# Performance work log

Hardware: AMD Instinct MI355X
Metric: run time of the kernel (lower is better)

## Reference

```python
import jax, jax.numpy as jnp
import numpy as np

HIDDEN = 2048
INTER = 5632
N_EXPERTS = 8
TOP_K = 2


def setup_inputs() -> dict:
    key = jax.random.key(0)
    ks = jax.random.split(key, 6)
    x = jax.random.normal(ks[0], (4, 2048, HIDDEN), dtype=jnp.float32)
    router_w = jax.random.normal(ks[1], (N_EXPERTS, HIDDEN), dtype=jnp.float32) * 0.02
    router_b = jnp.zeros((N_EXPERTS,), dtype=jnp.float32)
    Wg = jax.random.normal(ks[2], (N_EXPERTS, INTER, HIDDEN), dtype=jnp.float32) * 0.02
    Wu = jax.random.normal(ks[3], (N_EXPERTS, INTER, HIDDEN), dtype=jnp.float32) * 0.02
    Wd = jax.random.normal(ks[4], (N_EXPERTS, HIDDEN, INTER), dtype=jnp.float32) * 0.02
    return {"x": x, "router_w": router_w, "router_b": router_b, "Wg": Wg, "Wu": Wu, "Wd": Wd}


def reference(x, router_w, router_b, Wg, Wu, Wd):
    batch_shape = x.shape[:-1]
    xf = x.reshape(-1, HIDDEN)  # [T, H]
    T = xf.shape[0]

    # Router: softmax -> top-k -> renormalize (matches torch forward)
    logits = xf @ router_w.T + router_b            # [T, E]
    probs = jax.nn.softmax(logits, axis=-1)
    w, idx = jax.lax.top_k(probs, TOP_K)           # [T, K]
    w = w / jnp.sum(w, axis=-1, keepdims=True)

    # Dense combine weights [T, E]: zero where expert not selected.
    combine = jnp.zeros((T, N_EXPERTS), dtype=xf.dtype)
    combine = combine.at[jnp.arange(T)[:, None], idx].set(w)

    # Weighted sum of SwiGLU expert outputs (loop over fixed small E).
    out = jnp.zeros_like(xf)
    for e in range(N_EXPERTS):
        g = jax.nn.silu(xf @ Wg[e].T)              # [T, I]
        u = xf @ Wu[e].T                           # [T, I]
        h = (g * u) @ Wd[e].T                      # [T, H]
        out = out + combine[:, e:e + 1] * h
    return out.reshape(*batch_shape, HIDDEN)
```

## Files before the change

### kernel.cpp

```cpp
#include <hip/hip_runtime.h>
#include <stdint.h>

#define HID 2048
#define ITR 5632
#define NE 8
#define TT 8192

typedef __attribute__((ext_vector_type(4))) float f4;
typedef __attribute__((ext_vector_type(8))) short s8v;
typedef __attribute__((ext_vector_type(4))) float acc4;
typedef __attribute__((ext_vector_type(4))) unsigned short u4v;
typedef __attribute__((ext_vector_type(8))) unsigned short u8v;
typedef unsigned short ushort_t;

__device__ __forceinline__ unsigned short f2bf(float f) {
    union { float f; uint32_t u; } v; v.f = f;
    uint32_t u = v.u;
    return (unsigned short)((u + 0x7FFFu + ((u >> 16) & 1u)) >> 16);
}

__device__ __forceinline__ void gload16(const unsigned short* g, unsigned short* l) {
    __builtin_amdgcn_global_load_lds(
        (const __attribute__((address_space(1))) unsigned int*)g,
        (__attribute__((address_space(3))) unsigned int*)l, 16, 0, 0);
}

__device__ __forceinline__ int lby(int row, int s) {
    return row * 64 + ((s ^ ((row >> 1) & 3)) * 16);
}

__global__ __launch_bounds__(256) void k_cvt(const float* __restrict__ src,
                                             unsigned short* __restrict__ dst) {
    size_t i = ((size_t)blockIdx.x * 256 + threadIdx.x) * 8;
    f4 a = *(const f4*)(src + i);
    f4 b = *(const f4*)(src + i + 4);
    u8v o;
    o[0]=f2bf(a.x); o[1]=f2bf(a.y); o[2]=f2bf(a.z); o[3]=f2bf(a.w);
    o[4]=f2bf(b.x); o[5]=f2bf(b.y); o[6]=f2bf(b.z); o[7]=f2bf(b.w);
    *(u8v*)(dst + i) = o;
}

#define WBLK 45056
__global__ __launch_bounds__(256) void k_cvtW(const float* __restrict__ a,
                                              const float* __restrict__ b,
                                              const float* __restrict__ c,
                                              unsigned short* __restrict__ oa,
                                              unsigned short* __restrict__ ob,
                                              unsigned short* __restrict__ oc) {
    int bb = blockIdx.x;
    const float* s; unsigned short* d;
    if (bb < WBLK)            { s = a; d = oa; }
    else if (bb < 2 * WBLK)   { s = b; d = ob; bb -= WBLK; }
    else                      { s = c; d = oc; bb -= 2 * WBLK; }
    size_t i = ((size_t)bb * 256 + threadIdx.x) * 8;
    f4 va = *(const f4*)(s + i);
    f4 vb = *(const f4*)(s + i + 4);
    u8v o;
    o[0]=f2bf(va.x); o[1]=f2bf(va.y); o[2]=f2bf(va.z); o[3]=f2bf(va.w);
    o[4]=f2bf(vb.x); o[5]=f2bf(vb.y); o[6]=f2bf(vb.z); o[7]=f2bf(vb.w);
    *(u8v*)(d + i) = o;
}

__global__ __launch_bounds__(256) void k_router(const float* __restrict__ x,
                                                const float* __restrict__ rw,
                                                const float* __restrict__ rb,
                                                int* __restrict__ cnt,
                                                int* __restrict__ tokL,
                                                int* __restrict__ slotL,
                                                float* __restrict__ gateL) {
    int lane = threadIdx.x & 63;
    int wv = threadIdx.x >> 6;
    int t = blockIdx.x * 4 + wv;
    const float* xr = x + (size_t)t * HID;
    float acc[NE];
    #pragma unroll
    for (int e = 0; e < NE; ++e) acc[e] = 0.f;
    #pragma unroll
    for (int i = 0; i < 8; ++i) {
        f4 xv = *(const f4*)(xr + i * 256 + lane * 4);
        #pragma unroll
        for (int e = 0; e < NE; ++e) {
            f4 wv4 = *(const f4*)(rw + e * HID + i * 256 + lane * 4);
            acc[e] += xv.x * wv4.x + xv.y * wv4.y + xv.z * wv4.z + xv.w * wv4.w;
        }
    }
    #pragma unroll
    for (int off = 32; off; off >>= 1)
        #pragma unroll
        for (int e = 0; e < NE; ++e) acc[e] += __shfl_xor(acc[e], off, 64);
    if (lane == 0) {
        float lg[NE];
        #pragma unroll
        for (int e = 0; e < NE; ++e) lg[e] = acc[e] + rb[e];
        int i1 = 0;
        #pragma unroll
        for (int e = 1; e < NE; ++e) if (lg[e] > lg[i1]) i1 = e;
        int i2 = -1;
        #pragma unroll
        for (int e = 0; e < NE; ++e) {
            if (e == i1) continue;
            if (i2 < 0 || lg[e] > lg[i2]) i2 = e;
        }
        float ex = __expf(lg[i2] - lg[i1]);
        float w1 = 1.f / (1.f + ex);
        float w2 = ex / (1.f + ex);
        int p = atomicAdd(&cnt[i1], 1);
        tokL[i1 * TT + p] = t; slotL[i1 * TT + p] = t * 2;     gateL[i1 * TT + p] = w1;
        p = atomicAdd(&cnt[i2], 1);
        tokL[i2 * TT + p] = t; slotL[i2 * TT + p] = t * 2 + 1; gateL[i2 * TT + p] = w2;
    }
}


__global__ __launch_bounds__(512, 2) void k_g1p(const unsigned short* __restrict__ xb,
                                                const unsigned short* __restrict__ WgB,
                                                const unsigned short* __restrict__ WuB,
                                                const int* __restrict__ cnt,
                                                const int* __restrict__ tokL,
                                                const int* __restrict__ slotL,
                                                unsigned short* __restrict__ Hb) {
    int bx = blockIdx.x;
    int e = bx / (32 * 44);
    int r = bx % (32 * 44);
    int mt = r / 44, nt = r % 44;
    int M = cnt[e];
    int m0 = mt * 256;
    if (m0 >= M) return;
    int n0 = nt * 128;

    __shared__ __align__(16) unsigned short lds[65536];
    __shared__ int sTok[256];
    __shared__ int sSlot[256];

    int tid = threadIdx.x;
    if (tid < 256) {
        int m = m0 + tid;
        int mc = m < M ? m : M - 1;
        sTok[tid]  = tokL[e * TT + mc];
        sSlot[tid] = slotL[e * TT + mc];
    }
    __syncthreads();

    int wv = tid >> 6, lane = tid & 63;
    int lrow = lane >> 2;
    int slog = (lane & 3) ^ ((lane >> 3) & 3);

    const unsigned short* aS0 = xb + (size_t)sTok[(2 * wv) * 16 + lrow] * HID + slog * 8;
    const unsigned short* aS1 = xb + (size_t)sTok[(2 * wv + 1) * 16 + lrow] * HID + slog * 8;
    const unsigned short* gS  = WgB + ((size_t)e * ITR + n0 + wv * 16 + lrow) * HID + slog * 8;
    const unsigned short* uS  = WuB + ((size_t)e * ITR + n0 + wv * 16 + lrow) * HID + slog * 8;

    unsigned short* ldsA = lds;
    unsigned short* ldsG = lds + 32768;
    unsigned short* ldsU = lds + 49152;

    auto STAGE = [&](int reg, int kh) {
        int ko = kh * 32;
        gload16(aS0 + ko, ldsA + reg * 8192 + (2 * wv) * 512);
        gload16(aS1 + ko, ldsA + reg * 8192 + (2 * wv + 1) * 512);
        gload16(gS + ko,  ldsG + reg * 4096 + wv * 512);
        gload16(uS + ko,  ldsU + reg * 4096 + wv * 512);
    };

    int wr = wv >> 2, wc = wv & 3;
    int lr = lane & 15, ls = lane >> 4;

    int aOff[8], gOff[2], uOff[2];
    #pragma unroll
    for (int mi = 0; mi < 8; ++mi) aOff[mi] = lby(wr * 128 + mi * 16 + lr, ls);
    #pragma unroll
    for (int ni = 0; ni < 2; ++ni) {
        gOff[ni] = 65536 + lby(wc * 32 + ni * 16 + lr, ls);
        uOff[ni] = 98304 + lby(wc * 32 + ni * 16 + lr, ls);
    }

    acc4 zero4 = {0.f, 0.f, 0.f, 0.f};
    acc4 ag[8][2], au[8][2];
    #pragma unroll
    for (int mi = 0; mi < 8; ++mi)
        #pragma unroll
        for (int ni = 0; ni < 2; ++ni) { ag[mi][ni] = zero4; au[mi][ni] = zero4; }

    STAGE(0, 0); STAGE(1, 1); STAGE(2, 2); STAGE(3, 3);
    asm volatile("s_waitcnt vmcnt(12)" ::: "memory");
    __builtin_amdgcn_s_barrier();

    #pragma unroll 4
    for (int h = 0; h < 64; ++h) {
        int reg = h & 3;
        const char* baseA = (const char*)lds + reg * 16384;
        const char* baseB = (const char*)lds + reg * 8192;
        s8v af[8], gf[2], uf[2];
        #pragma unroll
        for (int mi = 0; mi < 8; ++mi) af[mi] = *(const s8v*)(baseA + aOff[mi]);
        #pragma unroll
        for (int ni = 0; ni < 2; ++ni) {
            gf[ni] = *(const s8v*)(baseB + gOff[ni]);
            uf[ni] = *(const s8v*)(baseB + uOff[ni]);
        }
        asm volatile("s_waitcnt lgkmcnt(0)" ::: "memory");
        __builtin_amdgcn_sched_barrier(0);
        __builtin_amdgcn_s_barrier();
        __builtin_amdgcn_sched_barrier(0);
        int kh = h + 4 < 64 ? h + 4 : 63;
        STAGE(reg, kh);
        __builtin_amdgcn_s_setprio(1);
        #pragma unroll
        for (int mi = 0; mi < 8; ++mi)
            #pragma unroll
            for (int ni = 0; ni < 2; ++ni) {
                ag[mi][ni] = __builtin_amdgcn_mfma_f32_16x16x32_bf16(af[mi], gf[ni], ag[mi][ni], 0, 0, 0);
                au[mi][ni] = __builtin_amdgcn_mfma_f32_16x16x32_bf16(af[mi], uf[ni], au[mi][ni], 0, 0, 0);
            }
        __builtin_amdgcn_s_setprio(0);
        asm volatile("s_waitcnt vmcnt(12)" ::: "memory");
        __builtin_amdgcn_s_barrier();
    }
    asm volatile("s_waitcnt vmcnt(0)" ::: "memory");

    #pragma unroll
    for (int mi = 0; mi < 8; ++mi) {
        #pragma unroll
        for (int j = 0; j < 4; ++j) {
            int m = wr * 128 + mi * 16 + ls * 4 + j;
            if (m0 + m < M) {
                size_t rowOff = (size_t)sSlot[m] * ITR + n0 + wc * 32 + lr;
                #pragma unroll
                for (int ni = 0; ni < 2; ++ni) {
                    float g = ag[mi][ni][j], u = au[mi][ni][j];
                    float h2 = g * (1.f / (1.f + __expf(-g))) * u;
                    Hb[rowOff + ni * 16] = f2bf(h2);
                }
            }
        }
    }
}

__global__ __launch_bounds__(512, 2) void k_g2p(const unsigned short* __restrict__ Hb,
                                                const unsigned short* __restrict__ WdB,
                                                const int* __restrict__ cnt,
                                                const int* __restrict__ tokL,
                                                const int* __restrict__ slotL,
                                                const float* __restrict__ gateL,
                                                float* __restrict__ out) {
    int bx = blockIdx.x;
    int e = bx / (32 * 8);
    int r = bx % (32 * 8);
    int mt = r / 8, nt = r % 8;
    int M = cnt[e];
    int m0 = mt * 256;
    if (m0 >= M) return;
    int n0 = nt * 256;

    __shared__ __align__(16) unsigned short lds[65536];
    __shared__ int sTok[256];
    __shared__ int sSlot[256];
    __shared__ float sGate[256];

    int tid = threadIdx.x;
    if (tid < 256) {
        int m = m0 + tid;
        int mc = m < M ? m : M - 1;
        sTok[tid]  = tokL[e * TT + mc];
        sSlot[tid] = slotL[e * TT + mc];
        sGate[tid] = gateL[e * TT + mc];
    }
    __syncthreads();

    int wv = tid >> 6, lane = tid & 63;
    int lrow = lane >> 2;
    int slog = (lane & 3) ^ ((lane >> 3) & 3);

    const unsigned short* aS0 = Hb + (size_t)sSlot[(2 * wv) * 16 + lrow] * ITR + slog * 8;
    const unsigned short* aS1 = Hb + (size_t)sSlot[(2 * wv + 1) * 16 + lrow] * ITR + slog * 8;
    const unsigned short* bS0 = WdB + ((size_t)e * HID + n0 + (2 * wv) * 16 + lrow) * ITR + slog * 8;
    const unsigned short* bS1 = WdB + ((size_t)e * HID + n0 + (2 * wv + 1) * 16 + lrow) * ITR + slog * 8;

    unsigned short* ldsA = lds;
    unsigned short* ldsB = lds + 32768;

    auto STAGE = [&](int reg, int kh) {
        int ko = kh * 32;
        gload16(aS0 + ko, ldsA + reg * 8192 + (2 * wv) * 512);
        gload16(aS1 + ko, ldsA + reg * 8192 + (2 * wv + 1) * 512);
        gload16(bS0 + ko, ldsB + reg * 8192 + (2 * wv) * 512);
        gload16(bS1 + ko, ldsB + reg * 8192 + (2 * wv + 1) * 512);
    };

    int wr = wv >> 2, wc = wv & 3;
    int lr = lane & 15, ls = lane >> 4;

    int aOff[8], bOff[4];
    #pragma unroll
    for (int mi = 0; mi < 8; ++mi) aOff[mi] = lby(wr * 128 + mi * 16 + lr, ls);
    #pragma unroll
    for (int ni = 0; ni < 4; ++ni) bOff[ni] = 65536 + lby(wc * 64 + ni * 16 + lr, ls);

    acc4 zero4 = {0.f, 0.f, 0.f, 0.f};
    acc4 a4[8][4];
    #pragma unroll
    for (int mi = 0; mi < 8; ++mi)
        #pragma unroll
        for (int ni = 0; ni < 4; ++ni) a4[mi][ni] = zero4;

    STAGE(0, 0); STAGE(1, 1); STAGE(2, 2); STAGE(3, 3);
    asm volatile("s_waitcnt vmcnt(12)" ::: "memory");
    __builtin_amdgcn_s_barrier();

    #pragma unroll 4
    for (int h = 0; h < 176; ++h) {
        int reg = h & 3;
        const char* base = (const char*)lds + reg * 16384;
        s8v af[8], bf[4];
        #pragma unroll
        for (int mi = 0; mi < 8; ++mi) af[mi] = *(const s8v*)(base + aOff[mi]);
        #pragma unroll
        for (int ni = 0; ni < 4; ++ni) bf[ni] = *(const s8v*)(base + bOff[ni]);
        asm volatile("s_waitcnt lgkmcnt(0)" ::: "memory");
        __builtin_amdgcn_sched_barrier(0);
        __builtin_amdgcn_s_barrier();
        __builtin_amdgcn_sched_barrier(0);
        int kh = h + 4 < 176 ? h + 4 : 175;
        STAGE(reg, kh);
        __builtin_amdgcn_s_setprio(1);
        #pragma unroll
        for (int mi = 0; mi < 8; ++mi)
            #pragma unroll
            for (int ni = 0; ni < 4; ++ni)
                a4[mi][ni] = __builtin_amdgcn_mfma_f32_16x16x32_bf16(af[mi], bf[ni], a4[mi][ni], 0, 0, 0);
        __builtin_amdgcn_s_setprio(0);
        asm volatile("s_waitcnt vmcnt(12)" ::: "memory");
        __builtin_amdgcn_s_barrier();
    }
    asm volatile("s_waitcnt vmcnt(0)" ::: "memory");

    #pragma unroll
    for (int mi = 0; mi < 8; ++mi) {
        #pragma unroll
        for (int j = 0; j < 4; ++j) {
            int m = wr * 128 + mi * 16 + ls * 4 + j;
            if (m0 + m < M) {
                int t = sTok[m];
                float w = sGate[m];
                float* orow = out + (size_t)t * HID + n0 + wc * 64 + lr;
                #pragma unroll
                for (int ni = 0; ni < 4; ++ni)
                    atomicAdd(orow + ni * 16, w * a4[mi][ni][j]);
            }
        }
    }
}

#define BM 128
#define BN 128
#define BK 64
#define MT1 64
#define NT1 44
#define NT2 16

__global__ __launch_bounds__(256) void k_gemm1(const unsigned short* __restrict__ xb,
                                               const float* __restrict__ Wg,
                                               const float* __restrict__ Wu,
                                               const int* __restrict__ cnt,
                                               const int* __restrict__ tokL,
                                               const int* __restrict__ slotL,
                                               unsigned short* __restrict__ Hb) {
    int bx = blockIdx.x;
    int e = bx / (MT1 * NT1);
    int r = bx % (MT1 * NT1);
    int mt = r / NT1, nt = r % NT1;
    int M = cnt[e];
    int m0 = mt * BM;
    if (m0 >= M) return;
    int n0 = nt * BN;

    __shared__ __align__(16) unsigned short lA[BM * BK];
    __shared__ __align__(16) unsigned short lBg[BN * BK];
    __shared__ __align__(16) unsigned short lBu[BN * BK];
    __shared__ int sTok[BM];
    __shared__ int sSlot[BM];

    int tid = threadIdx.x;
    if (tid < BM) {
        int m = m0 + tid;
        int mc = m < M ? m : M - 1;
        sTok[tid] = tokL[e * TT + mc];
        sSlot[tid] = slotL[e * TT + mc];
    }
    __syncthreads();

    int ar = tid >> 3, ac = tid & 7;
    const unsigned short* aP[4];
    #pragma unroll
    for (int i = 0; i < 4; ++i)
        aP[i] = xb + (size_t)sTok[ar + 32 * i] * HID + ac * 8;

    int br = tid >> 4, bc = tid & 15;
    const float* gB = Wg + ((size_t)e * ITR + n0) * HID + bc * 4;
    const float* uB = Wu + ((size_t)e * ITR + n0) * HID + bc * 4;

    int wv = tid >> 6, lane = tid & 63;
    int wm = (wv >> 1) * 64, wn = (wv & 1) * 64;
    int lr = lane & 15, lk = (lane >> 4) * 8;

    acc4 zero4 = {0.f, 0.f, 0.f, 0.f};
    acc4 ag[4][4], au[4][4];
    #pragma unroll
    for (int mi = 0; mi < 4; ++mi)
        #pragma unroll
        for (int ni = 0; ni < 4; ++ni) { ag[mi][ni] = zero4; au[mi][ni] = zero4; }

    for (int k0 = 0; k0 < HID; k0 += BK) {
        if (k0) __syncthreads();
        #pragma unroll
        for (int i = 0; i < 4; ++i) {
            int row = ar + 32 * i;
            s8v v = *(const s8v*)(aP[i] + k0);
            int byt = (row * 128 + ac * 16) ^ ((row & 7) << 4);
            *(s8v*)((char*)lA + byt) = v;
        }
        #pragma unroll
        for (int i = 0; i < 8; ++i) {
            int row = br + 16 * i;
            f4 vg = *(const f4*)(gB + (size_t)row * HID + k0);
            f4 vu = *(const f4*)(uB + (size_t)row * HID + k0);
            u4v og = { f2bf(vg.x), f2bf(vg.y), f2bf(vg.z), f2bf(vg.w) };
            u4v ou = { f2bf(vu.x), f2bf(vu.y), f2bf(vu.z), f2bf(vu.w) };
            int byt = (row * 128 + bc * 8) ^ ((row & 7) << 4);
            *(u4v*)((char*)lBg + byt) = og;
            *(u4v*)((char*)lBu + byt) = ou;
        }
        __syncthreads();
        #pragma unroll
        for (int kk = 0; kk < BK; kk += 32) {
            s8v af[4], gf[4], uf[4];
            #pragma unroll
            for (int i = 0; i < 4; ++i) {
                int rowA = wm + i * 16 + lr;
                af[i] = *(const s8v*)((char*)lA + ((rowA * 128 + (kk + lk) * 2) ^ ((rowA & 7) << 4)));
                int rowB = wn + i * 16 + lr;
                int bb = (rowB * 128 + (kk + lk) * 2) ^ ((rowB & 7) << 4);
                gf[i] = *(const s8v*)((char*)lBg + bb);
                uf[i] = *(const s8v*)((char*)lBu + bb);
            }
            #pragma unroll
            for (int mi = 0; mi < 4; ++mi)
                #pragma unroll
                for (int ni = 0; ni < 4; ++ni) {
                    ag[mi][ni] = __builtin_amdgcn_mfma_f32_16x16x32_bf16(af[mi], gf[ni], ag[mi][ni], 0, 0, 0);
                    au[mi][ni] = __builtin_amdgcn_mfma_f32_16x16x32_bf16(af[mi], uf[ni], au[mi][ni], 0, 0, 0);
                }
        }
    }
    #pragma unroll
    for (int mi = 0; mi < 4; ++mi) {
        #pragma unroll
        for (int j = 0; j < 4; ++j) {
            int m = wm + mi * 16 + (lane >> 4) * 4 + j;
            if (m0 + m < M) {
                size_t rowOff = (size_t)sSlot[m] * ITR + n0 + wn + lr;
                #pragma unroll
                for (int ni = 0; ni < 4; ++ni) {
                    float g = ag[mi][ni][j], u = au[mi][ni][j];
                    float h = g * (1.f / (1.f + __expf(-g))) * u;
                    Hb[rowOff + ni * 16] = f2bf(h);
                }
            }
        }
    }
}

__global__ __launch_bounds__(256) void k_gemm2(const unsigned short* __restrict__ Hb,
                                               const float* __restrict__ Wd,
                                               const int* __restrict__ cnt,
                                               const int* __restrict__ tokL,
                                               const int* __restrict__ slotL,
                                               const float* __restrict__ gateL,
                                               float* __restrict__ out) {
    int bx = blockIdx.x;
    int e = bx / (MT1 * NT2);
    int r = bx % (MT1 * NT2);
    int mt = r / NT2, nt = r % NT2;
    int M = cnt[e];
    int m0 = mt * BM;
    if (m0 >= M) return;
    int n0 = nt * BN;

    __shared__ __align__(16) unsigned short lA[BM * BK];
    __shared__ __align__(16) unsigned short lB[BN * BK];
    __shared__ int sTok[BM];
    __shared__ int sSlot[BM];
    __shared__ float sGate[BM];

    int tid = threadIdx.x;
    if (tid < BM) {
        int m = m0 + tid;
        int mc = m < M ? m : M - 1;
        sTok[tid] = tokL[e * TT + mc];
        sSlot[tid] = slotL[e * TT + mc];
        sGate[tid] = gateL[e * TT + mc];
    }
    __syncthreads();

    int ar = tid >> 3, ac = tid & 7;
    const unsigned short* aP[4];
    #pragma unroll
    for (int i = 0; i < 4; ++i)
        aP[i] = Hb + (size_t)sSlot[ar + 32 * i] * ITR + ac * 8;

    int br = tid >> 4, bc = tid & 15;
    const float* dB = Wd + ((size_t)e * HID + n0) * ITR + bc * 4;

    int wv = tid >> 6, lane = tid & 63;
    int wm = (wv >> 1) * 64, wn = (wv & 1) * 64;
    int lr = lane & 15, lk = (lane >> 4) * 8;

    acc4 zero4 = {0.f, 0.f, 0.f, 0.f};
    acc4 a4[4][4];
    #pragma unroll
    for (int mi = 0; mi < 4; ++mi)
        #pragma unroll
        for (int ni = 0; ni < 4; ++ni) a4[mi][ni] = zero4;

    for (int k0 = 0; k0 < ITR; k0 += BK) {
        if (k0) __syncthreads();
        #pragma unroll
        for (int i = 0; i < 4; ++i) {
            int row = ar + 32 * i;
            s8v v = *(const s8v*)(aP[i] + k0);
            int byt = (row * 128 + ac * 16) ^ ((row & 7) << 4);
            *(s8v*)((char*)lA + byt) = v;
        }
        #pragma unroll
        for (int i = 0; i < 8; ++i) {
            int row = br + 16 * i;
            f4 vd = *(const f4*)(dB + (size_t)row * ITR + k0);
            u4v od = { f2bf(vd.x), f2bf(vd.y), f2bf(vd.z), f2bf(vd.w) };
            int byt = (row * 128 + bc * 8) ^ ((row & 7) << 4);
            *(u4v*)((char*)lB + byt) = od;
        }
        __syncthreads();
        #pragma unroll
        for (int kk = 0; kk < BK; kk += 32) {
            s8v af[4], bf[4];
            #pragma unroll
            for (int i = 0; i < 4; ++i) {
                int rowA = wm + i * 16 + lr;
                af[i] = *(const s8v*)((char*)lA + ((rowA * 128 + (kk + lk) * 2) ^ ((rowA & 7) << 4)));
                int rowB = wn + i * 16 + lr;
                bf[i] = *(const s8v*)((char*)lB + ((rowB * 128 + (kk + lk) * 2) ^ ((rowB & 7) << 4)));
            }
            #pragma unroll
            for (int mi = 0; mi < 4; ++mi)
                #pragma unroll
                for (int ni = 0; ni < 4; ++ni)
                    a4[mi][ni] = __builtin_amdgcn_mfma_f32_16x16x32_bf16(af[mi], bf[ni], a4[mi][ni], 0, 0, 0);
        }
    }
    #pragma unroll
    for (int mi = 0; mi < 4; ++mi) {
        #pragma unroll
        for (int j = 0; j < 4; ++j) {
            int m = wm + mi * 16 + (lane >> 4) * 4 + j;
            if (m0 + m < M) {
                int t = sTok[m];
                float w = sGate[m];
                float* orow = out + (size_t)t * HID + n0 + wn + lr;
                #pragma unroll
                for (int ni = 0; ni < 4; ++ni)
                    atomicAdd(orow + ni * 16, w * a4[mi][ni][j]);
            }
        }
    }
}

extern "C" void kernel_launch(void* const* d_in, const int* in_sizes, int n_in,
                              void* d_out, int out_size, void* d_ws, size_t ws_size,
                              hipStream_t stream) {
    const float* x  = (const float*)d_in[0];
    const float* rw = (const float*)d_in[1];
    const float* rb = (const float*)d_in[2];
    const float* Wg = (const float*)d_in[3];
    const float* Wu = (const float*)d_in[4];
    const float* Wd = (const float*)d_in[5];
    float* out = (float*)d_out;
    char* ws = (char*)d_ws;

    const size_t OFF_XB   = 0;
    const size_t OFF_HB   = 33554432ull;
    const size_t OFF_TOK  = 218103808ull;
    const size_t OFF_SLOT = 218365952ull;
    const size_t OFF_GATE = 218628096ull;
    const size_t OFF_CNT  = 218890240ull;
    const size_t OFF_WG   = 218891264ull;
    const size_t OFF_WU   = 403440640ull;
    const size_t OFF_WD   = 587990016ull;
    const size_t NEED     = 772539392ull;

    unsigned short* xb   = (unsigned short*)(ws + OFF_XB);
    unsigned short* Hb   = (unsigned short*)(ws + OFF_HB);
    int*   tokL  = (int*)(ws + OFF_TOK);
    int*   slotL = (int*)(ws + OFF_SLOT);
    float* gateL = (float*)(ws + OFF_GATE);
    int*   cnt   = (int*)(ws + OFF_CNT);

    hipMemsetAsync(cnt, 0, NE * sizeof(int), stream);
    hipMemsetAsync(out, 0, (size_t)out_size * sizeof(float), stream);
    k_cvt<<<8192, 256, 0, stream>>>(x, xb);
    k_router<<<2048, 256, 0, stream>>>(x, rw, rb, cnt, tokL, slotL, gateL);

    if (ws_size >= NEED) {
        unsigned short* WgB = (unsigned short*)(ws + OFF_WG);
        unsigned short* WuB = (unsigned short*)(ws + OFF_WU);
        unsigned short* WdB = (unsigned short*)(ws + OFF_WD);
        k_cvtW<<<3 * WBLK, 256, 0, stream>>>(Wg, Wu, Wd, WgB, WuB, WdB);
        k_g1p<<<NE * 32 * 44, 512, 0, stream>>>(xb, WgB, WuB, cnt, tokL, slotL, Hb);
        k_g2p<<<NE * 32 * 8, 512, 0, stream>>>(Hb, WdB, cnt, tokL, slotL, gateL, out);
    } else {
        k_gemm1<<<NE * MT1 * NT1, 256, 0, stream>>>(xb, Wg, Wu, cnt, tokL, slotL, Hb);
        k_gemm2<<<NE * MT1 * NT2, 256, 0, stream>>>(Hb, Wd, cnt, tokL, slotL, gateL, out);
    }
}
```

Baseline: 1.938 ms.

## Restructure grouped-GEMM pipelines to single-barrier two-ahead prefetch without LDS swizzle

Reworks the k-loop in both grouped expert GEMM kernels. The old loop prefetched four stages ahead with two barriers per iteration. The new loop prefetches two stages ahead into a four-slot ring, issues global-to-LDS loads right after the fragment reads, and keeps one barrier per iteration, with the last two stages peeled out. It also drops the XOR swizzle on the LDS layout in favour of plain row-major offsets, which cuts address math but risks LDS bank conflicts on the fragment reads.

```diff
diff --git a/kernel.cpp b/kernel.cpp
--- a/kernel.cpp
+++ b/kernel.cpp
@@ -11,7 +11,6 @@
 typedef __attribute__((ext_vector_type(4))) float acc4;
 typedef __attribute__((ext_vector_type(4))) unsigned short u4v;
 typedef __attribute__((ext_vector_type(8))) unsigned short u8v;
-typedef unsigned short ushort_t;
 
 __device__ __forceinline__ unsigned short f2bf(float f) {
     union { float f; uint32_t u; } v; v.f = f;
@@ -25,9 +24,7 @@
         (__attribute__((address_space(3))) unsigned int*)l, 16, 0, 0);
 }
 
-__device__ __forceinline__ int lby(int row, int s) {
-    return row * 64 + ((s ^ ((row >> 1) & 3)) * 16);
-}
+#define MFMA16(a, b, c) __builtin_amdgcn_mfma_f32_16x16x32_bf16(a, b, c, 0, 0, 0)
 
 __global__ __launch_bounds__(256) void k_cvt(const float* __restrict__ src,
                                              unsigned short* __restrict__ dst) {
@@ -112,7 +109,7 @@
 }
 
 
-__global__ __launch_bounds__(512, 2) void k_g1p(const unsigned short* __restrict__ xb,
+__global__ __launch_bounds__(512, 2) void k_g1q(const unsigned short* __restrict__ xb,
                                                 const unsigned short* __restrict__ WgB,
                                                 const unsigned short* __restrict__ WuB,
                                                 const int* __restrict__ cnt,
@@ -128,7 +125,7 @@
     if (m0 >= M) return;
     int n0 = nt * 128;
 
-    __shared__ __align__(16) unsigned short lds[65536];
+    __shared__ __align__(16) unsigned short lds[4 * 16384];
     __shared__ int sTok[256];
     __shared__ int sSlot[256];
 
@@ -142,36 +139,24 @@
     __syncthreads();
 
     int wv = tid >> 6, lane = tid & 63;
-    int lrow = lane >> 2;
-    int slog = (lane & 3) ^ ((lane >> 3) & 3);
-
-    const unsigned short* aS0 = xb + (size_t)sTok[(2 * wv) * 16 + lrow] * HID + slog * 8;
-    const unsigned short* aS1 = xb + (size_t)sTok[(2 * wv + 1) * 16 + lrow] * HID + slog * 8;
-    const unsigned short* gS  = WgB + ((size_t)e * ITR + n0 + wv * 16 + lrow) * HID + slog * 8;
-    const unsigned short* uS  = WuB + ((size_t)e * ITR + n0 + wv * 16 + lrow) * HID + slog * 8;
-
-    unsigned short* ldsA = lds;
-    unsigned short* ldsG = lds + 32768;
-    unsigned short* ldsU = lds + 49152;
-
-    auto STAGE = [&](int reg, int kh) {
-        int ko = kh * 32;
-        gload16(aS0 + ko, ldsA + reg * 8192 + (2 * wv) * 512);
-        gload16(aS1 + ko, ldsA + reg * 8192 + (2 * wv + 1) * 512);
-        gload16(gS + ko,  ldsG + reg * 4096 + wv * 512);
-        gload16(uS + ko,  ldsU + reg * 4096 + wv * 512);
-    };
+    int srow = wv * 16 + (lane >> 2);
+    int scol = (lane & 3) * 8;
+    const unsigned short* sA0 = xb + (size_t)sTok[srow] * HID + scol;
+    const unsigned short* sA1 = xb + (size_t)sTok[128 + srow] * HID + scol;
+    const unsigned short* sG  = WgB + ((size_t)e * ITR + n0 + srow) * HID + scol;
+    const unsigned short* sU  = WuB + ((size_t)e * ITR + n0 + srow) * HID + scol;
+    int dstW = wv * 512;
 
     int wr = wv >> 2, wc = wv & 3;
     int lr = lane & 15, ls = lane >> 4;
 
     int aOff[8], gOff[2], uOff[2];
     #pragma unroll
-    for (int mi = 0; mi < 8; ++mi) aOff[mi] = lby(wr * 128 + mi * 16 + lr, ls);
+    for (int mi = 0; mi < 8; ++mi) aOff[mi] = (wr * 128 + mi * 16 + lr) * 32 + ls * 8;
     #pragma unroll
     for (int ni = 0; ni < 2; ++ni) {
-        gOff[ni] = 65536 + lby(wc * 32 + ni * 16 + lr, ls);
-        uOff[ni] = 98304 + lby(wc * 32 + ni * 16 + lr, ls);
+        gOff[ni] = 8192  + (wc * 32 + ni * 16 + lr) * 32 + ls * 8;
+        uOff[ni] = 12288 + (wc * 32 + ni * 16 + lr) * 32 + ls * 8;
     }
 
     acc4 zero4 = {0.f, 0.f, 0.f, 0.f};
@@ -181,42 +166,88 @@
         #pragma unroll
         for (int ni = 0; ni < 2; ++ni) { ag[mi][ni] = zero4; au[mi][ni] = zero4; }
 
-    STAGE(0, 0); STAGE(1, 1); STAGE(2, 2); STAGE(3, 3);
-    asm volatile("s_waitcnt vmcnt(12)" ::: "memory");
+    gload16(sA0,      lds + dstW);
+    gload16(sA1,      lds + 4096 + dstW);
+    gload16(sG,       lds + 8192 + dstW);
+    gload16(sU,       lds + 12288 + dstW);
+    gload16(sA0 + 32, lds + 16384 + dstW);
+    gload16(sA1 + 32, lds + 16384 + 4096 + dstW);
+    gload16(sG  + 32, lds + 16384 + 8192 + dstW);
+    gload16(sU  + 32, lds + 16384 + 12288 + dstW);
+    asm volatile("s_waitcnt vmcnt(4)" ::: "memory");
     __builtin_amdgcn_s_barrier();
-
+    __builtin_amdgcn_sched_barrier(0);
+
+    int kS = 64;
     #pragma unroll 4
-    for (int h = 0; h < 64; ++h) {
-        int reg = h & 3;
-        const char* baseA = (const char*)lds + reg * 16384;
-        const char* baseB = (const char*)lds + reg * 8192;
+    for (int tt = 0; tt < 62; ++tt) {
+        int base = (tt & 3) << 14;
         s8v af[8], gf[2], uf[2];
         #pragma unroll
-        for (int mi = 0; mi < 8; ++mi) af[mi] = *(const s8v*)(baseA + aOff[mi]);
+        for (int mi = 0; mi < 8; ++mi) af[mi] = *(const s8v*)(lds + base + aOff[mi]);
         #pragma unroll
         for (int ni = 0; ni < 2; ++ni) {
-            gf[ni] = *(const s8v*)(baseB + gOff[ni]);
-            uf[ni] = *(const s8v*)(baseB + uOff[ni]);
-        }
-        asm volatile("s_waitcnt lgkmcnt(0)" ::: "memory");
-        __builtin_amdgcn_sched_barrier(0);
+            gf[ni] = *(const s8v*)(lds + base + gOff[ni]);
+            uf[ni] = *(const s8v*)(lds + base + uOff[ni]);
+        }
+        int sb = ((tt + 2) & 3) << 14;
+        gload16(sA0 + kS, lds + sb + dstW);
+        gload16(sA1 + kS, lds + sb + 4096 + dstW);
+        gload16(sG  + kS, lds + sb + 8192 + dstW);
+        gload16(sU  + kS, lds + sb + 12288 + dstW);
+        kS += 32;
+        __builtin_amdgcn_s_setprio(1);
+        #pragma unroll
+        for (int mi = 0; mi < 8; ++mi)
+            #pragma unroll
+            for (int ni = 0; ni < 2; ++ni) {
+                ag[mi][ni] = MFMA16(af[mi], gf[ni], ag[mi][ni]);
+                au[mi][ni] = MFMA16(af[mi], uf[ni], au[mi][ni]);
+            }
+        __builtin_amdgcn_s_setprio(0);
+        asm volatile("s_waitcnt vmcnt(4)" ::: "memory");
         __builtin_amdgcn_s_barrier();
         __builtin_amdgcn_sched_barrier(0);
-        int kh = h + 4 < 64 ? h + 4 : 63;
-        STAGE(reg, kh);
-        __builtin_amdgcn_s_setprio(1);
+    }
+    {
+        int base = 2 << 14;
+        s8v af[8], gf[2], uf[2];
+        #pragma unroll
+        for (int mi = 0; mi < 8; ++mi) af[mi] = *(const s8v*)(lds + base + aOff[mi]);
+        #pragma unroll
+        for (int ni = 0; ni < 2; ++ni) {
+            gf[ni] = *(const s8v*)(lds + base + gOff[ni]);
+            uf[ni] = *(const s8v*)(lds + base + uOff[ni]);
+        }
         #pragma unroll
         for (int mi = 0; mi < 8; ++mi)
             #pragma unroll
             for (int ni = 0; ni < 2; ++ni) {
-                ag[mi][ni] = __builtin_amdgcn_mfma_f32_16x16x32_bf16(af[mi], gf[ni], ag[mi][ni], 0, 0, 0);
-                au[mi][ni] = __builtin_amdgcn_mfma_f32_16x16x32_bf16(af[mi], uf[ni], au[mi][ni], 0, 0, 0);
-            }
-        __builtin_amdgcn_s_setprio(0);
-        asm volatile("s_waitcnt vmcnt(12)" ::: "memory");
+                ag[mi][ni] = MFMA16(af[mi], gf[ni], ag[mi][ni]);
+                au[mi][ni] = MFMA16(af[mi], uf[ni], au[mi][ni]);
+            }
+        asm volatile("s_waitcnt vmcnt(0)" ::: "memory");
         __builtin_amdgcn_s_barrier();
-    }
-    asm volatile("s_waitcnt vmcnt(0)" ::: "memory");
+        __builtin_amdgcn_sched_barrier(0);
+    }
+    {
+        int base = 3 << 14;
+        s8v af[8], gf[2], uf[2];
+        #pragma unroll
+        for (int mi = 0; mi < 8; ++mi) af[mi] = *(const s8v*)(lds + base + aOff[mi]);
+        #pragma unroll
+        for (int ni = 0; ni < 2; ++ni) {
+            gf[ni] = *(const s8v*)(lds + base + gOff[ni]);
+            uf[ni] = *(const s8v*)(lds + base + uOff[ni]);
+        }
+        #pragma unroll
+        for (int mi = 0; mi < 8; ++mi)
+            #pragma unroll
+            for (int ni = 0; ni < 2; ++ni) {
+                ag[mi][ni] = MFMA16(af[mi], gf[ni], ag[mi][ni]);
+                au[mi][ni] = MFMA16(af[mi], uf[ni], au[mi][ni]);
+            }
+    }
 
     #pragma unroll
     for (int mi = 0; mi < 8; ++mi) {
@@ -228,15 +259,15 @@
                 #pragma unroll
                 for (int ni = 0; ni < 2; ++ni) {
                     float g = ag[mi][ni][j], u = au[mi][ni][j];
-                    float h2 = g * (1.f / (1.f + __expf(-g))) * u;
-                    Hb[rowOff + ni * 16] = f2bf(h2);
+                    float h = g * (1.f / (1.f + __expf(-g))) * u;
+                    Hb[rowOff + ni * 16] = f2bf(h);
                 }
             }
         }
     }
 }
 
-__global__ __launch_bounds__(512, 2) void k_g2p(const unsigned short* __restrict__ Hb,
+__global__ __launch_bounds__(512, 2) void k_g2q(const unsigned short* __restrict__ Hb,
                                                 const unsigned short* __restrict__ WdB,
                                                 const int* __restrict__ cnt,
                                                 const int* __restrict__ tokL,
@@ -252,7 +283,7 @@
     if (m0 >= M) return;
     int n0 = nt * 256;
 
-    __shared__ __align__(16) unsigned short lds[65536];
+    __shared__ __align__(16) unsigned short lds[4 * 16384];
     __shared__ int sTok[256];
     __shared__ int sSlot[256];
     __shared__ float sGate[256];
@@ -268,33 +299,22 @@
     __syncthreads();
 
     int wv = tid >> 6, lane = tid & 63;
-    int lrow = lane >> 2;
-    int slog = (lane & 3) ^ ((lane >> 3) & 3);
-
-    const unsigned short* aS0 = Hb + (size_t)sSlot[(2 * wv) * 16 + lrow] * ITR + slog * 8;
-    const unsigned short* aS1 = Hb + (size_t)sSlot[(2 * wv + 1) * 16 + lrow] * ITR + slog * 8;
-    const unsigned short* bS0 = WdB + ((size_t)e * HID + n0 + (2 * wv) * 16 + lrow) * ITR + slog * 8;
-    const unsigned short* bS1 = WdB + ((size_t)e * HID + n0 + (2 * wv + 1) * 16 + lrow) * ITR + slog * 8;
-
-    unsigned short* ldsA = lds;
-    unsigned short* ldsB = lds + 32768;
-
-    auto STAGE = [&](int reg, int kh) {
-        int ko = kh * 32;
-        gload16(aS0 + ko, ldsA + reg * 8192 + (2 * wv) * 512);
-        gload16(aS1 + ko, ldsA + reg * 8192 + (2 * wv + 1) * 512);
-        gload16(bS0 + ko, ldsB + reg * 8192 + (2 * wv) * 512);
-        gload16(bS1 + ko, ldsB + reg * 8192 + (2 * wv + 1) * 512);
-    };
+    int srow = wv * 16 + (lane >> 2);
+    int scol = (lane & 3) * 8;
+    const unsigned short* sH0 = Hb + (size_t)sSlot[srow] * ITR + scol;
+    const unsigned short* sH1 = Hb + (size_t)sSlot[128 + srow] * ITR + scol;
+    const unsigned short* sD0 = WdB + ((size_t)e * HID + n0 + srow) * ITR + scol;
+    const unsigned short* sD1 = WdB + ((size_t)e * HID + n0 + 128 + srow) * ITR + scol;
+    int dstW = wv * 512;
 
     int wr = wv >> 2, wc = wv & 3;
     int lr = lane & 15, ls = lane >> 4;
 
     int aOff[8], bOff[4];
     #pragma unroll
-    for (int mi = 0; mi < 8; ++mi) aOff[mi] = lby(wr * 128 + mi * 16 + lr, ls);
-    #pragma unroll
-    for (int ni = 0; ni < 4; ++ni) bOff[ni] = 65536 + lby(wc * 64 + ni * 16 + lr, ls);
+    for (int mi = 0; mi < 8; ++mi) aOff[mi] = (wr * 128 + mi * 16 + lr) * 32 + ls * 8;
+    #pragma unroll
+    for (int ni = 0; ni < 4; ++ni) bOff[ni] = 8192 + (wc * 64 + ni * 16 + lr) * 32 + ls * 8;
 
     acc4 zero4 = {0.f, 0.f, 0.f, 0.f};
     acc4 a4[8][4];
@@ -303,36 +323,73 @@
         #pragma unroll
         for (int ni = 0; ni < 4; ++ni) a4[mi][ni] = zero4;
 
-    STAGE(0, 0); STAGE(1, 1); STAGE(2, 2); STAGE(3, 3);
-    asm volatile("s_waitcnt vmcnt(12)" ::: "memory");
+    gload16(sH0,      lds + dstW);
+    gload16(sH1,      lds + 4096 + dstW);
+    gload16(sD0,      lds + 8192 + dstW);
+    gload16(sD1,      lds + 12288 + dstW);
+    gload16(sH0 + 32, lds + 16384 + dstW);
+    gload16(sH1 + 32, lds + 16384 + 4096 + dstW);
+    gload16(sD0 + 32, lds + 16384 + 8192 + dstW);
+    gload16(sD1 + 32, lds + 16384 + 12288 + dstW);
+    asm volatile("s_waitcnt vmcnt(4)" ::: "memory");
     __builtin_amdgcn_s_barrier();
-
+    __builtin_amdgcn_sched_barrier(0);
+
+    int kS = 64;
     #pragma unroll 4
-    for (int h = 0; h < 176; ++h) {
-        int reg = h & 3;
-        const char* base = (const char*)lds + reg * 16384;
+    for (int tt = 0; tt < 174; ++tt) {
+        int base = (tt & 3) << 14;
         s8v af[8], bf[4];
         #pragma unroll
-        for (int mi = 0; mi < 8; ++mi) af[mi] = *(const s8v*)(base + aOff[mi]);
-        #pragma unroll
-        for (int ni = 0; ni < 4; ++ni) bf[ni] = *(const s8v*)(base + bOff[ni]);
-        asm volatile("s_waitcnt lgkmcnt(0)" ::: "memory");
-        __builtin_amdgcn_sched_barrier(0);
+        for (int mi = 0; mi < 8; ++mi) af[mi] = *(const s8v*)(lds + base + aOff[mi]);
+        #pragma unroll
+        for (int ni = 0; ni < 4; ++ni) bf[ni] = *(const s8v*)(lds + base + bOff[ni]);
+        int sb = ((tt + 2) & 3) << 14;
+        gload16(sH0 + kS, lds + sb + dstW);
+        gload16(sH1 + kS, lds + sb + 4096 + dstW);
+        gload16(sD0 + kS, lds + sb + 8192 + dstW);
+        gload16(sD1 + kS, lds + sb + 12288 + dstW);
+        kS += 32;
+        __builtin_amdgcn_s_setprio(1);
+        #pragma unroll
+        for (int mi = 0; mi < 8; ++mi)
+            #pragma unroll
+            for (int ni = 0; ni < 4; ++ni)
+                a4[mi][ni] = MFMA16(af[mi], bf[ni], a4[mi][ni]);
+        __builtin_amdgcn_s_setprio(0);
+        asm volatile("s_waitcnt vmcnt(4)" ::: "memory");
         __builtin_amdgcn_s_barrier();
         __builtin_amdgcn_sched_barrier(0);
-        int kh = h + 4 < 176 ? h + 4 : 175;
-        STAGE(reg, kh);
-        __builtin_amdgcn_s_setprio(1);
+    }
+    {
+        int base = 2 << 14;
+        s8v af[8], bf[4];
+        #pragma unroll
+        for (int mi = 0; mi < 8; ++mi) af[mi] = *(const s8v*)(lds + base + aOff[mi]);
+        #pragma unroll
+        for (int ni = 0; ni < 4; ++ni) bf[ni] = *(const s8v*)(lds + base + bOff[ni]);
         #pragma unroll
         for (int mi = 0; mi < 8; ++mi)
             #pragma unroll
             for (int ni = 0; ni < 4; ++ni)
-                a4[mi][ni] = __builtin_amdgcn_mfma_f32_16x16x32_bf16(af[mi], bf[ni], a4[mi][ni], 0, 0, 0);
-        __builtin_amdgcn_s_setprio(0);
-        asm volatile("s_waitcnt vmcnt(12)" ::: "memory");
+                a4[mi][ni] = MFMA16(af[mi], bf[ni], a4[mi][ni]);
+        asm volatile("s_waitcnt vmcnt(0)" ::: "memory");
         __builtin_amdgcn_s_barrier();
-    }
-    asm volatile("s_waitcnt vmcnt(0)" ::: "memory");
+        __builtin_amdgcn_sched_barrier(0);
+    }
+    {
+        int base = 3 << 14;
+        s8v af[8], bf[4];
+        #pragma unroll
+        for (int mi = 0; mi < 8; ++mi) af[mi] = *(const s8v*)(lds + base + aOff[mi]);
+        #pragma unroll
+        for (int ni = 0; ni < 4; ++ni) bf[ni] = *(const s8v*)(lds + base + bOff[ni]);
+        #pragma unroll
+        for (int mi = 0; mi < 8; ++mi)
+            #pragma unroll
+            for (int ni = 0; ni < 4; ++ni)
+                a4[mi][ni] = MFMA16(af[mi], bf[ni], a4[mi][ni]);
+    }
 
     #pragma unroll
     for (int mi = 0; mi < 8; ++mi) {
@@ -447,8 +504,8 @@
             for (int mi = 0; mi < 4; ++mi)
                 #pragma unroll
                 for (int ni = 0; ni < 4; ++ni) {
-                    ag[mi][ni] = __builtin_amdgcn_mfma_f32_16x16x32_bf16(af[mi], gf[ni], ag[mi][ni], 0, 0, 0);
-                    au[mi][ni] = __builtin_amdgcn_mfma_f32_16x16x32_bf16(af[mi], uf[ni], au[mi][ni], 0, 0, 0);
+                    ag[mi][ni] = MFMA16(af[mi], gf[ni], ag[mi][ni]);
+                    au[mi][ni] = MFMA16(af[mi], uf[ni], au[mi][ni]);
                 }
         }
     }
@@ -554,7 +611,7 @@
             for (int mi = 0; mi < 4; ++mi)
                 #pragma unroll
                 for (int ni = 0; ni < 4; ++ni)
-                    a4[mi][ni] = __builtin_amdgcn_mfma_f32_16x16x32_bf16(af[mi], bf[ni], a4[mi][ni], 0, 0, 0);
+                    a4[mi][ni] = MFMA16(af[mi], bf[ni], a4[mi][ni]);
         }
     }
     #pragma unroll
@@ -614,8 +671,8 @@
         unsigned short* WuB = (unsigned short*)(ws + OFF_WU);
         unsigned short* WdB = (unsigned short*)(ws + OFF_WD);
         k_cvtW<<<3 * WBLK, 256, 0, stream>>>(Wg, Wu, Wd, WgB, WuB, WdB);
-        k_g1p<<<NE * 32 * 44, 512, 0, stream>>>(xb, WgB, WuB, cnt, tokL, slotL, Hb);
-        k_g2p<<<NE * 32 * 8, 512, 0, stream>>>(Hb, WdB, cnt, tokL, slotL, gateL, out);
+        k_g1q<<<NE * 32 * 44, 512, 0, stream>>>(xb, WgB, WuB, cnt, tokL, slotL, Hb);
+        k_g2q<<<NE * 32 * 8, 512, 0, stream>>>(Hb, WdB, cnt, tokL, slotL, gateL, out);
     } else {
         k_gemm1<<<NE * MT1 * NT1, 256, 0, stream>>>(xb, Wg, Wu, cnt, tokL, slotL, Hb);
         k_gemm2<<<NE * MT1 * NT2, 256, 0, stream>>>(Hb, Wd, cnt, tokL, slotL, gateL, out);
```

Measured after the change: 1.988 ms. 1.03x slower.
